# Kernel optimization log

Hardware: AMD Instinct MI355X
Metric: run time of the kernel (lower is better)

## Reference

```python
import jax, jax.numpy as jnp
import numpy as np
from jax import lax

K = 32768          # queue size
C = 100            # num_classes == len(cls_num_list1)
B = 1024           # batch size (features.shape[0] - K)
D = 128            # embedding dim
ALPHA = 0.05; BETA = 1.0; GAMMA = 1.0; SUPT = 1.0
T = 0.07; BASE_T = 0.07   # base_temperature defaults to temperature
SMOOTH = 0.0; EPS = 1e-12


def setup_inputs() -> dict:
    key = jax.random.key(0)
    k1, k2, k3, k4 = jax.random.split(key, 4)
    features = jax.random.normal(k1, (B + K, D), dtype=jnp.float32)
    features = features / jnp.linalg.norm(features, axis=1, keepdims=True)  # contrastive feats are L2-normalized
    centers = jax.random.normal(k2, (C, D), dtype=jnp.float32)
    centers = centers / jnp.linalg.norm(centers, axis=1, keepdims=True)
    sup_logits = jax.random.normal(k3, (B, C), dtype=jnp.float32)
    labels = jax.random.randint(k4, (B + K,), 0, C, dtype=jnp.int32)
    return {"features": features, "sup_logits": sup_logits, "centers": centers, "labels": labels}


def _loss(features, sup_logits, centers, labels):
    f32 = features.dtype
    lab_c = jnp.arange(C, dtype=labels.dtype)
    lab1 = jnp.concatenate([labels[:B], lab_c])                 # [B+C]
    mask = (labels[:B, None] == labels[None, :]).astype(f32)    # [B, B+K]
    mask1 = (lab1[:B, None] == lab1[None, :]).astype(f32)       # [B, B+C]
    # class counts over batch+queue (batch_cls_count) and batch+centers (batch_cls_count1)
    cls_count = jnp.zeros((C,), f32).at[labels].add(1.0)
    cls_count1 = jnp.zeros((C,), f32).at[lab1].add(1.0)
    diag = jnp.arange(B)
    logits_mask = jnp.ones((B, B + K), f32).at[diag, diag].set(0.0)
    logits_mask1 = jnp.ones((B, B + C), f32).at[diag, diag].set(0.0)
    mask = mask * logits_mask
    mask1 = mask1 * logits_mask1

    # ---- branch 1: batch anchors vs [batch, class centers] ----
    feats1 = jnp.concatenate([features[:B], centers], axis=0)   # [B+C, D]
    logits1 = (features[:B] @ feats1.T) / T                     # [B, B+C]
    logits1 = logits1 - lax.stop_gradient(logits1.max(axis=1, keepdims=True))
    exp1 = jnp.exp(logits1) * logits_mask1
    w1 = cls_count1[lab1][None, :] - mask1                      # per-instance class weight
    denom1 = (exp1 / w1).sum(axis=1, keepdims=True)
    log_prob1 = logits1 - jnp.log(denom1 + EPS)
    loss1 = -jnp.mean((mask1 * log_prob1).sum(1) / mask1.sum(1))

    # ---- branch 2: [sup_logits, batch anchors vs batch+queue] ----
    adc = (features[:B] @ features.T) / T                       # [B, B+K]
    logits = jnp.concatenate([sup_logits / SUPT, adc], axis=1)  # [B, C+B+K] (self.weight is None)
    logits = logits - lax.stop_gradient(logits.max(axis=1, keepdims=True))
    one_hot = jax.nn.one_hot(labels[:B], C, dtype=f32)
    one_hot = SMOOTH / (C - 1) * (1.0 - one_hot) + (1.0 - SMOOTH) * one_hot
    mask_full = jnp.concatenate([one_hot * BETA, mask * ALPHA], axis=1)
    lmask_full = jnp.concatenate([jnp.ones((B, C), f32), GAMMA * logits_mask], axis=1)
    expl = jnp.exp(logits) * lmask_full
    lab_full = jnp.concatenate([lab_c, labels])                 # [C+B+K]
    w = cls_count[lab_full][None, :] - mask_full
    denom = (expl / w).sum(axis=1, keepdims=True)
    log_prob = logits - jnp.log(denom + EPS)
    loss2 = -(T / BASE_T) * jnp.mean((mask_full * log_prob).sum(1) / mask_full.sum(1))
    return loss1 + loss2


def reference(features, sup_logits, centers, labels):
    return _loss(features, sup_logits, centers, labels)
```

## Files before the change

### kernel.cpp

```cpp
#include <hip/hip_runtime.h>
#include <math.h>

#define KQ   32768
#define CC   100
#define BB   1024
#define DD   128
#define NTOT (BB + KQ)
#define CB_CENT 1056
#define NCB  1060
#define NPT  1088
#define NHIST 33
#define NCG2 132
#define CG_SUP 141
#define NSL  141

#define INV_T  14.285714285714286f
#define K2E    20.609929f
#define ALPHA  0.05f
#define EPSV   1e-12f

typedef __attribute__((ext_vector_type(8)))  short          short8;
typedef __attribute__((ext_vector_type(8)))  unsigned short ushort8;
typedef __attribute__((ext_vector_type(16))) float          float16;

__device__ __forceinline__ unsigned short f2bf_rne(float f) {
    unsigned int u = __float_as_uint(f);
    return (unsigned short)((u + 0x7FFFu + ((u >> 16) & 1u)) >> 16);
}

__device__ __forceinline__ void glds16(const void* g, void* l) {
    __builtin_amdgcn_global_load_lds(
        (const __attribute__((address_space(1))) void*)g,
        (__attribute__((address_space(3))) void*)l, 16, 0, 0);
}


__global__ __launch_bounds__(256) void prep_k(const float* __restrict__ feats,
                                              const float* __restrict__ centers,
                                              const int* __restrict__ labels,
                                              unsigned short* __restrict__ X2,
                                              int* __restrict__ cntP,
                                              int* __restrict__ cntB) {
    const int b = blockIdx.x, t = threadIdx.x;
    if (b >= NPT) {
        const int h = b - NPT;
        __shared__ int hA[CC], hB[CC];
        if (t < CC) { hA[t] = 0; hB[t] = 0; }
        __syncthreads();
        const int base = h * 1024;
#pragma unroll
        for (int q = 0; q < 4; ++q) {
            int l = labels[base + q * 256 + t];
            atomicAdd(&hA[l], 1);
            if (h == 0) atomicAdd(&hB[l], 1);
        }
        __syncthreads();
        if (t < 128) {
            cntP[h * 128 + t] = (t < CC) ? hA[t] : 0;
            if (h == 0) cntB[t] = (t < CC) ? hB[t] : 0;
        }
        return;
    }
    const int x = b & 7, i = b >> 3;
    const int cg_ = x + 8 * (i >> 3);
    const int cb = cg_ * 8 + (i & 7);
    if (cb >= NCB) return;
    __shared__ unsigned short sm[8 * 66 * 8];
    const int rl = t >> 3, c8 = t & 7;
    const int r = cb * 32 + rl;
    const float* src;
    if (r < NTOT)            src = &feats[(size_t)r * DD];
    else if (r < NTOT + CC)  src = &centers[(size_t)(r - NTOT) * DD];
    else                     src = nullptr;
#pragma unroll
    for (int s = 0; s < 2; ++s) {
        const int c8p = c8 + 8 * s;
        float v[8];
        if (src) {
            const float4* p = (const float4*)(src + c8p * 8);
            float4 q0 = p[0], q1 = p[1];
            v[0]=q0.x; v[1]=q0.y; v[2]=q0.z; v[3]=q0.w;
            v[4]=q1.x; v[5]=q1.y; v[6]=q1.z; v[7]=q1.w;
        } else {
#pragma unroll
            for (int j = 0; j < 8; ++j) v[j] = 0.f;
        }
        ushort8 H;
#pragma unroll
        for (int m = 0; m < 8; ++m) H[m] = f2bf_rne(v[m]);
        const int ks = c8p >> 1, lh = c8p & 1;
        *(ushort8*)&sm[(ks * 66 + rl + 32 * lh) * 8] = H;
    }
    __syncthreads();
    ushort8* dst = (ushort8*)((char*)X2 + (size_t)cb * 8192);
#pragma unroll
    for (int j = 0; j < 2; ++j) {
        const int idx = j * 256 + t;
        const int ks = idx >> 6, ln2 = idx & 63;
        dst[idx] = *(const ushort8*)&sm[(ks * 66 + ln2) * 8];
    }
}

__device__ __forceinline__ void epi_tile(
    const float16& acc, int cb, int lc, float rn, float drm, bool checkDiag,
    int half, int ln, int growbase, const int* rlab, float* sS, float* sN)
{
    const int ccol = cb * 32 + ln;
#pragma unroll
    for (int reg = 0; reg < 16; ++reg) {
        int ro = (reg & 3) + 8 * (reg >> 2) + 4 * half;
        float a  = acc[reg];
        float mf = (lc == rlab[reg]) ? 1.f : 0.f;
        float wgt = fmaf(mf, drm, rn);
        if (checkDiag) {
            bool d = (ccol == growbase + ro);
            wgt = d ? 0.f : wgt;
            mf  = d ? 0.f : mf;
        }
        float e = exp2f(fmaf(a, K2E, -K2E));
        sS[reg] = fmaf(e, wgt, sS[reg]);
        sN[reg] = fmaf(mf, a, sN[reg]);
    }
}

__global__ __launch_bounds__(256, 2) void gemm_k(
    const unsigned short* __restrict__ X2, const int* __restrict__ labels,
    const int* __restrict__ cntP, const int* __restrict__ cntB,
    const float* __restrict__ sup,
    float* __restrict__ pS, float* __restrict__ pN,
    float* __restrict__ supS, float* __restrict__ supLi) {
    const int b = blockIdx.x;
    const int xcd = b & 7, rgrp = (b >> 3) & 7, chunk = b >> 6;
    const int cg = chunk * 8 + xcd;
    if (cg > CG_SUP) return;

    const int tid = threadIdx.x;
    const int w = tid >> 6, lane = tid & 63;
    const int half = lane >> 5, ln = lane & 31;
    const int rb = rgrp * 4 + w;
    const char* Xb = (const char*)X2;

    if (cg == CG_SUP) {
        const int c0 = lane, c1 = lane + 64;
        int s0 = 0, s1 = 0;
#pragma unroll
        for (int h = 0; h < NHIST; ++h) {
            s0 += cntP[h * 128 + c0];
            s1 += cntP[h * 128 + c1];
        }
        float n0 = (float)s0;
        float rA0 = __builtin_amdgcn_rcpf(n0);
        float rAm0 = __builtin_amdgcn_rcpf(fmaxf(n0 - 1.f, 1.f));
        float rA1 = 0.f, rAm1 = 0.f;
        if (lane < 36) {
            float n1 = (float)s1;
            rA1 = __builtin_amdgcn_rcpf(n1);
            rAm1 = __builtin_amdgcn_rcpf(fmaxf(n1 - 1.f, 1.f));
        }
        for (int rr = 0; rr < 32; ++rr) {
            int row = rb * 32 + rr;
            int li = labels[row];
            const float* srow = &sup[(size_t)row * CC];
            float v0 = srow[c0];
            float s = __expf(v0 - INV_T) * ((c0 == li) ? rAm0 : rA0);
            float liv = (c0 == li) ? v0 : 0.f;
            if (lane < 36) {
                float v1 = srow[c1];
                s += __expf(v1 - INV_T) * ((c1 == li) ? rAm1 : rA1);
                liv += (c1 == li) ? v1 : 0.f;
            }
#pragma unroll
            for (int off = 1; off < 64; off <<= 1) {
                s += __shfl_xor(s, off, 64);
                liv += __shfl_xor(liv, off, 64);
            }
            if (lane == 0) { supS[row] = s; supLi[row] = liv; }
        }
        return;
    }

    __shared__ char sm[2 * 8192];
    __shared__ float2 wT[128];

    const bool isB2 = (cg < NCG2);
    const int t1 = cg - NCG2;
    const bool isBatch = isB2 || (t1 < 8);
    const int NIT = isB2 ? 8 : 4;
    const int cb0 = isB2 ? cg * 8 : (t1 < 8 ? t1 * 4 : CB_CENT);

    if (tid < 128) {
        int s = 0;
#pragma unroll
        for (int h = 0; h < NHIST; ++h) s += cntP[h * 128 + tid];
        float2 wv;
        if (isB2) {
            float cf = (float)s;
            float rn = (s > 0) ? __builtin_amdgcn_rcpf(cf) : 0.f;
            wv = make_float2(rn, (s > 0) ? (__builtin_amdgcn_rcpf(cf - ALPHA) - rn) : 0.f);
        } else {
            float c1 = (float)(cntB[tid] + 1);
            float r1 = __builtin_amdgcn_rcpf(c1);
            wv = make_float2(r1, __builtin_amdgcn_rcpf(fmaxf(c1 - 1.f, 1.f)) - r1);
        }
        wT[tid] = wv;
    }

    const int wbase = w * 2048;
    {
        const char* src = Xb + (size_t)cb0 * 8192 + wbase + lane * 16;
        glds16(src, &sm[wbase]);
        glds16(src + 1024, &sm[wbase + 1024]);
    }

    int lcv[8];
#pragma unroll
    for (int i = 0; i < 8; ++i) {
        if (i < NIT) {
            const int cb = cb0 + i;
            if (isBatch) {
                lcv[i] = labels[cb * 32 + ln];
            } else {
                int q = cb * 32 + ln - NTOT;
                lcv[i] = (q < CC) ? q : -1;
            }
        } else lcv[i] = -1;
    }

    const int growbase = rb * 32;
    short8 Ah[8];
    {
        size_t abase = (size_t)rb * 8192 + (size_t)lane * 16;
#pragma unroll
        for (int ks = 0; ks < 8; ++ks)
            Ah[ks] = *(const short8*)(Xb + abase + (size_t)ks * 1024);
    }
    int rlab[16];
#pragma unroll
    for (int reg = 0; reg < 16; ++reg) {
        int ro = (reg & 3) + 8 * (reg >> 2) + 4 * half;
        rlab[reg] = labels[growbase + ro];
    }

    __syncthreads();

    float rnv[8], drv[8];
#pragma unroll
    for (int i = 0; i < 8; ++i) {
        if (i < NIT) {
            int lc = lcv[i];
            float2 wv = wT[(lc >= 0) ? lc : 0];
            rnv[i] = (lc >= 0) ? wv.x : 0.f;
            drv[i] = (lc >= 0) ? wv.y : 0.f;
        } else { rnv[i] = 0.f; drv[i] = 0.f; }
    }

    float sS[16], sN[16];
#pragma unroll
    for (int reg = 0; reg < 16; ++reg) { sS[reg] = 0.f; sN[reg] = 0.f; }

    for (int i = 0; i < NIT; ++i) {
        const int cb = cb0 + i;
        const bool more = (i + 1 < NIT);
        if (more) {
            const char* src = Xb + (size_t)(cb + 1) * 8192 + wbase + lane * 16;
            char* dl = &sm[((i + 1) & 1) * 8192 + wbase];
            glds16(src, dl);
            glds16(src + 1024, dl + 1024);
        }
        const char* Bp = &sm[(i & 1) * 8192 + lane * 16];
        float16 a;
#pragma unroll
        for (int reg = 0; reg < 16; ++reg) a[reg] = 0.f;
#pragma unroll
        for (int ks = 0; ks < 8; ++ks) {
            short8 Bf = *(const short8*)(Bp + ks * 1024);
            a = __builtin_amdgcn_mfma_f32_32x32x16_bf16(Ah[ks], Bf, a, 0, 0, 0);
        }
        epi_tile(a, cb, lcv[i], rnv[i], drv[i], isBatch && (cb == rb),
                 half, ln, growbase, rlab, sS, sN);
        __syncthreads();
    }

    const int slice = isB2 ? cg : (NCG2 + t1);
#pragma unroll
    for (int reg = 0; reg < 16; ++reg) {
        float av = sS[reg], c = sN[reg];
#pragma unroll
        for (int off = 1; off < 32; off <<= 1) {
            av += __shfl_xor(av, off, 64);
            c  += __shfl_xor(c, off, 64);
        }
        if (ln == 0) {
            int ro = (reg & 3) + 8 * (reg >> 2) + 4 * half;
            int grow = growbase + ro;
            pS[(size_t)slice * BB + grow] = av;
            pN[(size_t)slice * BB + grow] = c;
        }
    }
}

__global__ __launch_bounds__(256) void reduce_k(
    const int* __restrict__ labels,
    const int* __restrict__ cntP, const int* __restrict__ cntB,
    const float* __restrict__ pS, const float* __restrict__ pN,
    const float* __restrict__ supS, const float* __restrict__ supLi,
    float* __restrict__ partial) {
    const int g = blockIdx.x, t = threadIdx.x;
    __shared__ float cA_s[128];
    __shared__ int   cB_s[128];
    if (t < 128) {
        int s = 0;
#pragma unroll
        for (int h = 0; h < NHIST; ++h) s += cntP[h * 128 + t];
        cA_s[t] = (float)s;
        cB_s[t] = cntB[t];
    }
    __syncthreads();
    const int rl = t >> 5, j = t & 31;
    const int row = g * 8 + rl;
    float S2 = 0.f, N2 = 0.f, S1 = 0.f, N1v = 0.f;
    for (int c = j; c < NCG2; c += 32) {
        S2 += pS[(size_t)c * BB + row];
        N2 += pN[(size_t)c * BB + row];
    }
    if (NCG2 + j < NSL) {
        S1  += pS[(size_t)(NCG2 + j) * BB + row];
        N1v += pN[(size_t)(NCG2 + j) * BB + row];
    }
#pragma unroll
    for (int off = 1; off < 32; off <<= 1) {
        S2 += __shfl_xor(S2, off, 64);  N2  += __shfl_xor(N2, off, 64);
        S1 += __shfl_xor(S1, off, 64);  N1v += __shfl_xor(N1v, off, 64);
    }
    float s = 0.f;
    if (j == 0) {
        int li = labels[row];
        S2 += supS[row];
        N2 *= INV_T; N1v *= INV_T;
        float sli = supLi[row];
        float cA = cA_s[li];
        float msum2 = fmaf(ALPHA, cA - 1.f, 1.f);
        float loss2 = -(fmaf(ALPHA, N2, sli) / msum2 - INV_T - logf(S2 + EPSV));
        float loss1 = -(N1v / (float)cB_s[li] - INV_T - logf(S1 + EPSV));
        s = loss1 + loss2;
    }
#pragma unroll
    for (int off = 1; off < 64; off <<= 1) s += __shfl_xor(s, off, 64);
    __shared__ float buf[4];
    if ((t & 63) == 0) buf[t >> 6] = s;
    __syncthreads();
    if (t == 0) partial[g] = (buf[0] + buf[1]) + (buf[2] + buf[3]);
}

__global__ __launch_bounds__(64) void final_k(const float* __restrict__ partial,
                                              float* __restrict__ out) {
    const int t = threadIdx.x;
    float s = partial[t] + partial[t + 64];
#pragma unroll
    for (int off = 1; off < 64; off <<= 1) s += __shfl_xor(s, off, 64);
    if (t == 0) out[0] = s / (float)BB;
}

extern "C" void kernel_launch(void* const* d_in, const int* in_sizes, int n_in,
                              void* d_out, int out_size, void* d_ws, size_t ws_size,
                              hipStream_t stream) {
    const float* feats   = (const float*)d_in[0];
    const float* sup     = (const float*)d_in[1];
    const float* centers = (const float*)d_in[2];
    const int*   labels  = (const int*)d_in[3];
    float* out = (float*)d_out;
    char*  wsb = (char*)d_ws;

    const size_t X2_BYTES = (size_t)NCB * 8192;
    unsigned short* X2 = (unsigned short*)wsb;
    char* base2 = wsb + X2_BYTES;
    int* cntP = (int*)base2;
    int* cntB = cntP + NHIST * 128;
    float* pS = (float*)(cntB + 128);
    float* pN = pS + (size_t)NSL * BB;
    float* supS  = pN + (size_t)NSL * BB;
    float* supLi = supS + BB;
    float* partial = supLi + BB;

    prep_k<<<NPT + NHIST, 256, 0, stream>>>(feats, centers, labels, X2, cntP, cntB);
    gemm_k<<<18 * 64, 256, 0, stream>>>(X2, labels, cntP, cntB, sup,
                                        pS, pN, supS, supLi);
    reduce_k<<<128, 256, 0, stream>>>(labels, cntP, cntB, pS, pN, supS, supLi, partial);
    final_k<<<1, 64, 0, stream>>>(partial, out);
}
```

Before: 122.0 us.

## Triple-buffer B tiles with manual waitcnt barriers and packed-FMA epilogue

Changes the LDS staging of B tiles from double to triple buffering, prefetching two tiles ahead. The full __syncthreads is replaced by explicit vmcnt waits plus s_barrier. The epilogue and final reduction now use 2-wide float vectors so the compiler can emit packed FMA, and the partial sums are written as float2. The aim is to hide global-to-LDS latency and cut epilogue ALU cost, at the price of more LDS per block, which may reduce occupancy, and hand-written waitcnt logic that must stay correct.

New measurement: 128.8 us. 1.06x slower.

```diff
diff --git a/kernel.cpp b/kernel.cpp
--- a/kernel.cpp
+++ b/kernel.cpp
@@ -22,6 +22,7 @@
 typedef __attribute__((ext_vector_type(8)))  short          short8;
 typedef __attribute__((ext_vector_type(8)))  unsigned short ushort8;
 typedef __attribute__((ext_vector_type(16))) float          float16;
+typedef __attribute__((ext_vector_type(2)))  float          f32x2;
 
 __device__ __forceinline__ unsigned short f2bf_rne(float f) {
     unsigned int u = __float_as_uint(f);
@@ -103,23 +104,32 @@
 
 __device__ __forceinline__ void epi_tile(
     const float16& acc, int cb, int lc, float rn, float drm, bool checkDiag,
-    int half, int ln, int growbase, const int* rlab, float* sS, float* sN)
+    int half, int ln, int growbase, const int* rlab, f32x2* sS, f32x2* sN)
 {
     const int ccol = cb * 32 + ln;
 #pragma unroll
-    for (int reg = 0; reg < 16; ++reg) {
-        int ro = (reg & 3) + 8 * (reg >> 2) + 4 * half;
-        float a  = acc[reg];
-        float mf = (lc == rlab[reg]) ? 1.f : 0.f;
-        float wgt = fmaf(mf, drm, rn);
+    for (int pr = 0; pr < 8; ++pr) {
+        const int r0 = 2 * pr;
+        const int ro0 = (r0 & 3) + 8 * (r0 >> 2) + 4 * half;
+        f32x2 av;  av.x = acc[r0];  av.y = acc[r0 + 1];
+        f32x2 mfv;
+        mfv.x = (lc == rlab[r0])     ? 1.f : 0.f;
+        mfv.y = (lc == rlab[r0 + 1]) ? 1.f : 0.f;
+        f32x2 drm2; drm2.x = drm; drm2.y = drm;
+        f32x2 rn2;  rn2.x = rn;  rn2.y = rn;
+        f32x2 wgt = __builtin_elementwise_fma(mfv, drm2, rn2);
         if (checkDiag) {
-            bool d = (ccol == growbase + ro);
-            wgt = d ? 0.f : wgt;
-            mf  = d ? 0.f : mf;
-        }
-        float e = exp2f(fmaf(a, K2E, -K2E));
-        sS[reg] = fmaf(e, wgt, sS[reg]);
-        sN[reg] = fmaf(mf, a, sN[reg]);
+            bool d0 = (ccol == growbase + ro0);
+            bool d1 = (ccol == growbase + ro0 + 1);
+            wgt.x = d0 ? 0.f : wgt.x;  wgt.y = d1 ? 0.f : wgt.y;
+            mfv.x = d0 ? 0.f : mfv.x;  mfv.y = d1 ? 0.f : mfv.y;
+        }
+        f32x2 k2; k2.x = K2E; k2.y = K2E;
+        f32x2 nk; nk.x = -K2E; nk.y = -K2E;
+        f32x2 ex = __builtin_elementwise_fma(av, k2, nk);
+        f32x2 e;  e.x = exp2f(ex.x);  e.y = exp2f(ex.y);
+        sS[pr] = __builtin_elementwise_fma(e, wgt, sS[pr]);
+        sN[pr] = __builtin_elementwise_fma(mfv, av, sN[pr]);
     }
 }
 
@@ -179,7 +189,7 @@
         return;
     }
 
-    __shared__ char sm[2 * 8192];
+    __shared__ char sm[3 * 8192];
     __shared__ float2 wT[128];
 
     const bool isB2 = (cg < NCG2);
@@ -205,13 +215,6 @@
         wT[tid] = wv;
     }
 
-    const int wbase = w * 2048;
-    {
-        const char* src = Xb + (size_t)cb0 * 8192 + wbase + lane * 16;
-        glds16(src, &sm[wbase]);
-        glds16(src + 1024, &sm[wbase + 1024]);
-    }
-
     int lcv[8];
 #pragma unroll
     for (int i = 0; i < 8; ++i) {
@@ -241,7 +244,19 @@
         rlab[reg] = labels[growbase + ro];
     }
 
-    __syncthreads();
+    const int wbase = w * 2048;
+    __builtin_amdgcn_sched_barrier(0);
+    {
+        const char* s0p = Xb + (size_t)cb0 * 8192 + wbase + lane * 16;
+        glds16(s0p, &sm[wbase]);
+        glds16(s0p + 1024, &sm[wbase + 1024]);
+        const char* s1p = Xb + (size_t)(cb0 + 1) * 8192 + wbase + lane * 16;
+        glds16(s1p, &sm[8192 + wbase]);
+        glds16(s1p + 1024, &sm[8192 + wbase + 1024]);
+    }
+    asm volatile("s_waitcnt lgkmcnt(0) vmcnt(2)" ::: "memory");
+    __builtin_amdgcn_s_barrier();
+    __builtin_amdgcn_sched_barrier(0);
 
     float rnv[8], drv[8];
 #pragma unroll
@@ -254,20 +269,21 @@
         } else { rnv[i] = 0.f; drv[i] = 0.f; }
     }
 
-    float sS[16], sN[16];
-#pragma unroll
-    for (int reg = 0; reg < 16; ++reg) { sS[reg] = 0.f; sN[reg] = 0.f; }
+    f32x2 sS[8], sN[8];
+#pragma unroll
+    for (int pr = 0; pr < 8; ++pr) {
+        sS[pr].x = 0.f; sS[pr].y = 0.f; sN[pr].x = 0.f; sN[pr].y = 0.f;
+    }
 
     for (int i = 0; i < NIT; ++i) {
         const int cb = cb0 + i;
-        const bool more = (i + 1 < NIT);
-        if (more) {
-            const char* src = Xb + (size_t)(cb + 1) * 8192 + wbase + lane * 16;
-            char* dl = &sm[((i + 1) & 1) * 8192 + wbase];
+        if (i + 2 < NIT) {
+            const char* src = Xb + (size_t)(cb + 2) * 8192 + wbase + lane * 16;
+            char* dl = &sm[((i + 2) % 3) * 8192 + wbase];
             glds16(src, dl);
             glds16(src + 1024, dl + 1024);
         }
-        const char* Bp = &sm[(i & 1) * 8192 + lane * 16];
+        const char* Bp = &sm[(i % 3) * 8192 + lane * 16];
         float16 a;
 #pragma unroll
         for (int reg = 0; reg < 16; ++reg) a[reg] = 0.f;
@@ -278,23 +294,34 @@
         }
         epi_tile(a, cb, lcv[i], rnv[i], drv[i], isBatch && (cb == rb),
                  half, ln, growbase, rlab, sS, sN);
-        __syncthreads();
+        if (i + 1 < NIT) {
+            if (i + 2 < NIT) asm volatile("s_waitcnt vmcnt(2)" ::: "memory");
+            else             asm volatile("s_waitcnt vmcnt(0)" ::: "memory");
+            __builtin_amdgcn_s_barrier();
+            __builtin_amdgcn_sched_barrier(0);
+        }
     }
 
     const int slice = isB2 ? cg : (NCG2 + t1);
 #pragma unroll
-    for (int reg = 0; reg < 16; ++reg) {
-        float av = sS[reg], c = sN[reg];
+    for (int pr = 0; pr < 8; ++pr) {
+        f32x2 av = sS[pr], cv = sN[pr];
 #pragma unroll
         for (int off = 1; off < 32; off <<= 1) {
-            av += __shfl_xor(av, off, 64);
-            c  += __shfl_xor(c, off, 64);
+            f32x2 tv;
+            tv.x = __shfl_xor(av.x, off, 64);
+            tv.y = __shfl_xor(av.y, off, 64);
+            av += tv;
+            tv.x = __shfl_xor(cv.x, off, 64);
+            tv.y = __shfl_xor(cv.y, off, 64);
+            cv += tv;
         }
         if (ln == 0) {
-            int ro = (reg & 3) + 8 * (reg >> 2) + 4 * half;
-            int grow = growbase + ro;
-            pS[(size_t)slice * BB + grow] = av;
-            pN[(size_t)slice * BB + grow] = c;
+            const int r0 = 2 * pr;
+            const int ro0 = (r0 & 3) + 8 * (r0 >> 2) + 4 * half;
+            const int g0 = growbase + ro0;
+            *(float2*)&pS[(size_t)slice * BB + g0] = make_float2(av.x, av.y);
+            *(float2*)&pN[(size_t)slice * BB + g0] = make_float2(cv.x, cv.y);
         }
     }
 }
```
